# Performance work log

Measured on AMD Instinct MI355X. Metric: run time of the kernel, lower is better.

The kernel has to match this reference:

```python
import jax, jax.numpy as jnp
import numpy as np

B, N_LAT, N_CTX, DIM = 4, 512, 4096, 512
HEADS, DIM_HEAD = 8, 64
DIM_INNER = HEADS * DIM_HEAD  # 512


def setup_inputs() -> dict:
    key = jax.random.key(0)
    k1, k2, k3, k4, k5 = jax.random.split(key, 5)
    x = jax.random.normal(k1, (B, N_LAT, DIM), dtype=jnp.float32)
    context = jax.random.normal(k2, (B, N_CTX, DIM), dtype=jnp.float32)
    # eqx.nn.Linear weights have shape (out_features, in_features); scale ~ 1/sqrt(in)
    s = 1.0 / np.sqrt(DIM)
    Wq = jax.random.normal(k3, (DIM_INNER, DIM), dtype=jnp.float32) * s
    Wkv = jax.random.normal(k4, (2 * DIM_INNER, DIM), dtype=jnp.float32) * s
    Wout = jax.random.normal(k5, (DIM, DIM_INNER), dtype=jnp.float32) * (1.0 / np.sqrt(DIM_INNER))
    return {"x": x, "context": context, "Wq": Wq, "Wkv": Wkv, "Wout": Wout}


def reference(x, context, Wq, Wkv, Wout):
    h, d = HEADS, DIM_HEAD
    # queries are prepended to the context (unconditional in the source)
    ctx = jnp.concatenate([x, context], axis=1)              # [b, n+m, dim]
    q = jnp.einsum('bnd,ed->bne', x, Wq)                     # [b, n, h*d]
    kv = jnp.einsum('bmd,ed->bme', ctx, Wkv)                 # [b, n+m, 2*h*d]
    k, v = jnp.split(kv, 2, axis=-1)
    # b n (h d) -> b h n d
    def split_heads(t):
        b, n, _ = t.shape
        return t.reshape(b, n, h, d).transpose(0, 2, 1, 3)
    q, k, v = split_heads(q), split_heads(k), split_heads(v)
    scale = d ** (-0.5)
    scores = jnp.einsum('bhnd,bhmd->bhnm', q, k) * scale     # [b, h, n, n+m]
    attn = jax.nn.softmax(scores, axis=-1)
    out = jnp.einsum('bhnm,bhmd->bhnd', attn, v)             # [b, h, n, d]
    b, _, n, _ = out.shape
    out = out.transpose(0, 2, 1, 3).reshape(b, n, h * d)     # b h n d -> b n (h d)
    return jnp.einsum('bne,de->bnd', out, Wout)
```

## Files before the change

kernel.cpp:

```cpp
#include <hip/hip_runtime.h>
#include <hip/hip_bf16.h>
#include <cstdint>

#define DEVI __device__ __forceinline__

typedef unsigned short u16;
typedef unsigned int u32;
typedef __attribute__((ext_vector_type(8))) short bf16x8;
typedef __attribute__((ext_vector_type(4))) float f32x4;
typedef __attribute__((ext_vector_type(4))) int i32x4;

DEVI u16 f2bf(float f) {
    union { float f; u32 u; } v; v.f = f;
    u32 r = v.u + 0x7fffu + ((v.u >> 16) & 1u);
    return (u16)(r >> 16);
}
DEVI u32 pk2(float a, float b) { return (u32)f2bf(a) | ((u32)f2bf(b) << 16); }

DEVI u32 cvtpk_bf16(float lo, float hi) {
    u32 r;
    asm("v_cvt_pk_bf16_f32 %0, %1, %2" : "=v"(r) : "v"(lo), "v"(hi));
    return r;
}

DEVI void gload_lds16(const void* g, void* l) {
    __builtin_amdgcn_global_load_lds(
        (const __attribute__((address_space(1))) u32*)(uintptr_t)g,
        (__attribute__((address_space(3))) u32*)(u32)(uintptr_t)l,
        16, 0, 0);
}

__global__ __launch_bounds__(256) void prep_all(const float* __restrict__ x,
                                                const float* __restrict__ ctx,
                                                const float* __restrict__ Wq,
                                                const float* __restrict__ Wkv,
                                                const float* __restrict__ Wout,
                                                u16* __restrict__ ctxb,
                                                u16* __restrict__ wqb,
                                                u16* __restrict__ wkvb,
                                                u16* __restrict__ woutb) {
    int id = blockIdx.x;
    int tid = threadIdx.x;
    if (id < 4608) {
        int idx = id * 256 + tid;
        long e0 = (long)idx * 8;
        int b = (int)(e0 / (4608L * 512));
        long rem = e0 % (4608L * 512);
        int m = (int)(rem / 512);
        int d = (int)(rem % 512);
        const float* src = (m < 512) ? (x + ((long)b * 512 + m) * 512 + d)
                                     : (ctx + ((long)b * 4096 + (m - 512)) * 512 + d);
        float4 a = *(const float4*)src;
        float4 c = *(const float4*)(src + 4);
        uint4 u;
        u.x = pk2(a.x, a.y); u.y = pk2(a.z, a.w);
        u.z = pk2(c.x, c.y); u.w = pk2(c.z, c.w);
        *(uint4*)&ctxb[e0] = u;
        return;
    }
    const float* s;
    u16* d;
    int i;
    if (id < 4736)      { s = Wq;   d = wqb;   i = (id - 4608) * 256 + tid; }
    else if (id < 4992) { s = Wkv;  d = wkvb;  i = (id - 4736) * 256 + tid; }
    else                { s = Wout; d = woutb; i = (id - 4992) * 256 + tid; }
    const float4* s4 = (const float4*)s;
    float4 a = s4[i * 2], b = s4[i * 2 + 1];
    uint4 u;
    u.x = pk2(a.x, a.y); u.y = pk2(a.z, a.w);
    u.z = pk2(b.x, b.y); u.w = pk2(b.z, b.w);
    ((uint4*)d)[i] = u;
}

__global__ __launch_bounds__(512) void gemm_kvq(const u16* __restrict__ ctxb,
                                                const u16* __restrict__ wkvb,
                                                const u16* __restrict__ wqb,
                                                u16* __restrict__ kb,
                                                u16* __restrict__ vtb,
                                                u16* __restrict__ qb) {
    const int K = 512;
    __shared__ u16 Asm[2][128 * 64];
    __shared__ u16 Bsm[2][256 * 64];
    int tid = threadIdx.x;
    int w = tid >> 6, l = tid & 63;
    int g = l >> 4, c = l & 15;
    int wr = w >> 2, wc = w & 3;

    const u16* B;
    u16* C;
    long r0, arow0;
    int rpb;
    bool isq = (blockIdx.y >= 144);
    if (isq) {
        if (blockIdx.x >= 2) return;
        r0 = (long)(blockIdx.y - 144) * 128;
        rpb = 512;
        B = wqb;
        C = qb;
    } else {
        r0 = (long)blockIdx.y * 128;
        rpb = 4608;
        B = wkvb;
        C = kb;
    }
    arow0 = (r0 / rpb) * (4608L * 512) + (r0 % rpb) * K;
    int n0 = blockIdx.x * 256;

    f32x4 acc[4][4];
#pragma unroll
    for (int i = 0; i < 4; i++)
#pragma unroll
        for (int j = 0; j < 4; j++) acc[i][j] = (f32x4){0.f, 0.f, 0.f, 0.f};

    int srow = l >> 3;
    int sch = l & 7;

    auto stage = [&](int kt, int bb) {
#pragma unroll
        for (int i = 0; i < 2; i++) {
            int c2 = w * 2 + i;
            int row = c2 * 8 + srow;
            int sc = sch ^ (row & 7);
            gload_lds16(ctxb + arow0 + (long)row * K + kt * 64 + sc * 8,
                        &Asm[bb][c2 * 512 + (l << 3)]);
        }
#pragma unroll
        for (int i = 0; i < 4; i++) {
            int c2 = w * 4 + i;
            int row = c2 * 8 + srow;
            int sc = sch ^ (row & 7);
            gload_lds16(B + (long)(n0 + row) * K + kt * 64 + sc * 8,
                        &Bsm[bb][c2 * 512 + (l << 3)]);
        }
    };

    stage(0, 0);
#pragma unroll 2
    for (int kt = 0; kt < 8; ++kt) {
        int pb = kt & 1;
        if (kt < 7) {
            stage(kt + 1, pb ^ 1);
            asm volatile("s_waitcnt vmcnt(6)" ::: "memory");
        } else {
            asm volatile("s_waitcnt vmcnt(0)" ::: "memory");
        }
        __builtin_amdgcn_s_barrier();
        __builtin_amdgcn_sched_barrier(0);
#pragma unroll
        for (int ks = 0; ks < 2; ++ks) {
            bf16x8 af[4], bfr[4];
#pragma unroll
            for (int mt = 0; mt < 4; ++mt) {
                int row = wr * 64 + mt * 16 + c;
                int ch = (ks * 4 + g) ^ (row & 7);
                af[mt] = *(const bf16x8*)&Asm[pb][row * 64 + ch * 8];
            }
#pragma unroll
            for (int nt = 0; nt < 4; ++nt) {
                int row = wc * 64 + nt * 16 + c;
                int ch = (ks * 4 + g) ^ (row & 7);
                bfr[nt] = *(const bf16x8*)&Bsm[pb][row * 64 + ch * 8];
            }
            __builtin_amdgcn_s_setprio(1);
#pragma unroll
            for (int mt = 0; mt < 4; ++mt)
#pragma unroll
                for (int nt = 0; nt < 4; ++nt)
                    acc[mt][nt] = __builtin_amdgcn_mfma_f32_16x16x32_bf16(
                        af[mt], bfr[nt], acc[mt][nt], 0, 0, 0);
            __builtin_amdgcn_s_setprio(0);
        }
        __builtin_amdgcn_s_barrier();
    }

    if (!isq && n0 >= 512) {
        int b2 = (int)(r0 / 4608);
        int mb = (int)(r0 - (long)b2 * 4608) + wr * 64;
#pragma unroll
        for (int mt = 0; mt < 4; ++mt) {
#pragma unroll
            for (int nt = 0; nt < 4; ++nt) {
                int colv = (n0 - 512) + wc * 64 + nt * 16 + c;
                int hh = colv >> 6, dd = colv & 63;
                long ob = ((long)(b2 * 8 + hh) * 64 + dd) * 4608 + mb + mt * 16 + g * 4;
                ushort4 pk;
                pk.x = f2bf(acc[mt][nt][0]);
                pk.y = f2bf(acc[mt][nt][1]);
                pk.z = f2bf(acc[mt][nt][2]);
                pk.w = f2bf(acc[mt][nt][3]);
                *(ushort4*)&vtb[ob] = pk;
            }
        }
        return;
    }
#pragma unroll
    for (int mt = 0; mt < 4; ++mt) {
#pragma unroll
        for (int r = 0; r < 4; ++r) {
            long row = r0 + wr * 64 + mt * 16 + g * 4 + r;
#pragma unroll
            for (int nt = 0; nt < 4; ++nt) {
                int col = n0 + wc * 64 + nt * 16 + c;
                C[row * 512 + col] = f2bf(acc[mt][nt][r]);
            }
        }
    }
}

__global__ __launch_bounds__(256) void gemm_out(const u16* __restrict__ A,
                                                const u16* __restrict__ B,
                                                float* __restrict__ C) {
    const int K = 512;
    __shared__ u16 Asm[2][64 * 64];
    __shared__ u16 Bsm[2][128 * 64];
    int tid = threadIdx.x;
    int w = tid >> 6, l = tid & 63;
    int g = l >> 4, c = l & 15;
    int wr = w >> 1, wc = w & 1;
    long r0 = (long)blockIdx.y * 64;
    long arow0 = r0 * K;
    int n0 = blockIdx.x * 128;

    f32x4 acc[2][4];
#pragma unroll
    for (int i = 0; i < 2; i++)
#pragma unroll
        for (int j = 0; j < 4; j++) acc[i][j] = (f32x4){0.f, 0.f, 0.f, 0.f};

    int srow = l >> 3;
    int sch = l & 7;

    auto stage = [&](int kt, int bb) {
#pragma unroll
        for (int i = 0; i < 2; i++) {
            int c2 = w * 2 + i;
            int row = c2 * 8 + srow;
            int sc = sch ^ (row & 7);
            gload_lds16(A + arow0 + (long)row * K + kt * 64 + sc * 8,
                        &Asm[bb][c2 * 512 + (l << 3)]);
        }
#pragma unroll
        for (int i = 0; i < 4; i++) {
            int c2 = w * 4 + i;
            int row = c2 * 8 + srow;
            int sc = sch ^ (row & 7);
            gload_lds16(B + (long)(n0 + row) * K + kt * 64 + sc * 8,
                        &Bsm[bb][c2 * 512 + (l << 3)]);
        }
    };

    stage(0, 0);
#pragma unroll 2
    for (int kt = 0; kt < 8; ++kt) {
        int pb = kt & 1;
        if (kt < 7) {
            stage(kt + 1, pb ^ 1);
            asm volatile("s_waitcnt vmcnt(6)" ::: "memory");
        } else {
            asm volatile("s_waitcnt vmcnt(0)" ::: "memory");
        }
        __builtin_amdgcn_s_barrier();
        __builtin_amdgcn_sched_barrier(0);
#pragma unroll
        for (int ks = 0; ks < 2; ++ks) {
            bf16x8 af[2], bfr[4];
#pragma unroll
            for (int mt = 0; mt < 2; ++mt) {
                int row = wr * 32 + mt * 16 + c;
                int ch = (ks * 4 + g) ^ (row & 7);
                af[mt] = *(const bf16x8*)&Asm[pb][row * 64 + ch * 8];
            }
#pragma unroll
            for (int nt = 0; nt < 4; ++nt) {
                int row = wc * 64 + nt * 16 + c;
                int ch = (ks * 4 + g) ^ (row & 7);
                bfr[nt] = *(const bf16x8*)&Bsm[pb][row * 64 + ch * 8];
            }
#pragma unroll
            for (int mt = 0; mt < 2; ++mt)
#pragma unroll
                for (int nt = 0; nt < 4; ++nt)
                    acc[mt][nt] = __builtin_amdgcn_mfma_f32_16x16x32_bf16(
                        af[mt], bfr[nt], acc[mt][nt], 0, 0, 0);
        }
        __builtin_amdgcn_s_barrier();
    }
#pragma unroll
    for (int mt = 0; mt < 2; ++mt) {
#pragma unroll
        for (int r = 0; r < 4; ++r) {
            long row = r0 + wr * 32 + mt * 16 + g * 4 + r;
#pragma unroll
            for (int nt = 0; nt < 4; ++nt) {
                int col = n0 + wc * 64 + nt * 16 + c;
                C[row * 512 + col] = acc[mt][nt][r];
            }
        }
    }
}

__global__ __launch_bounds__(256) void attn_kern(const u16* __restrict__ Q,
                                                 const u16* __restrict__ KB,
                                                 const u16* __restrict__ VT,
                                                 float* __restrict__ Op,
                                                 float2* __restrict__ ML) {
    __shared__ u16 Ksm[2][64 * 64];
    __shared__ u16 Vsm[2][64 * 64];
    int tid = threadIdx.x;
    int w = tid >> 6, l = tid & 63;
    int g = l >> 4, c = l & 15;
    int id = blockIdx.x;
    int u = (id & 7) | ((id >> 6) << 3);
    int qi = (id >> 3) & 7;
    int p_ = u >> 3, chunk = u & 7;
    int b = p_ >> 3, h = p_ & 7;
    int qb0 = qi * 64;
    const int NT = 9;
    int it0 = chunk * NT;

    bf16x8 qf[2];
    {
        long qrow = (long)(b * 512 + qb0 + w * 16 + c);
#pragma unroll
        for (int ks = 0; ks < 2; ++ks)
            qf[ks] = *(const bf16x8*)&Q[qrow * 512 + h * 64 + ks * 32 + g * 8];
    }
    f32x4 o[4];
#pragma unroll
    for (int nt = 0; nt < 4; nt++) o[nt] = (f32x4){0.f, 0.f, 0.f, 0.f};
    float mrun = -1e30f, lrun = 0.f;

    const float SCL = 0.125f * 1.44269504f;
    int srow8 = l >> 3, sch = l & 7;
    const long kbase = (long)b * 4608 * 512 + h * 64;
    const long vtbase = (long)(b * 8 + h) * 64 * 4608;

    int g2 = g << 1;
    int srcA = ((g2 & 3) << 4) | c;
    int srcB = (((g2 | 1) & 3) << 4) | c;
    bool hiT2 = (g >> 1) != 0;

    auto stage = [&](int it, int bb) {
#pragma unroll
        for (int i = 0; i < 2; i++) {
            int c2 = w * 2 + i;
            int row = c2 * 8 + srow8;
            int sc = sch ^ (row & 7);
            gload_lds16(KB + kbase + (long)(it * 64 + row) * 512 + sc * 8,
                        &Ksm[bb][c2 * 512 + (l << 3)]);
            gload_lds16(VT + vtbase + (long)row * 4608 + it * 64 + sc * 8,
                        &Vsm[bb][c2 * 512 + (l << 3)]);
        }
    };

    stage(it0, 0);
    for (int t = 0; t < NT; ++t) {
        int pbuf = t & 1;
        if (t + 1 < NT) {
            stage(it0 + t + 1, pbuf ^ 1);
            asm volatile("s_waitcnt vmcnt(4)" ::: "memory");
        } else {
            asm volatile("s_waitcnt vmcnt(0)" ::: "memory");
        }
        __builtin_amdgcn_s_barrier();
        __builtin_amdgcn_sched_barrier(0);

        f32x4 st[4];
#pragma unroll
        for (int t2 = 0; t2 < 4; t2++) st[t2] = (f32x4){0.f, 0.f, 0.f, 0.f};
        __builtin_amdgcn_s_setprio(1);
#pragma unroll
        for (int ks = 0; ks < 2; ++ks) {
#pragma unroll
            for (int t2 = 0; t2 < 4; t2++) {
                int row = t2 * 16 + c;
                int ch = (ks * 4 + g) ^ (row & 7);
                bf16x8 kf = *(const bf16x8*)&Ksm[pbuf][row * 64 + ch * 8];
                st[t2] = __builtin_amdgcn_mfma_f32_16x16x32_bf16(kf, qf[ks], st[t2], 0, 0, 0);
            }
        }
        __builtin_amdgcn_s_setprio(0);

        float mx01 = fmaxf(fmaxf(st[0][0], st[0][1]), fmaxf(st[0][2], st[0][3]));
        float mx23 = fmaxf(fmaxf(st[1][0], st[1][1]), fmaxf(st[1][2], st[1][3]));
        float mx45 = fmaxf(fmaxf(st[2][0], st[2][1]), fmaxf(st[2][2], st[2][3]));
        float mx67 = fmaxf(fmaxf(st[3][0], st[3][1]), fmaxf(st[3][2], st[3][3]));
        float mx = fmaxf(fmaxf(mx01, mx23), fmaxf(mx45, mx67)) * SCL;
        mx = fmaxf(mx, __shfl_xor(mx, 16));
        mx = fmaxf(mx, __shfl_xor(mx, 32));

        bool need = mx > mrun + 8.f;
        if (__ballot(need)) {
            float mnew = fmaxf(mrun, mx);
            float rf = exp2f(mrun - mnew);
            mrun = mnew;
            lrun *= rf;
#pragma unroll
            for (int nt = 0; nt < 4; nt++)
#pragma unroll
                for (int r = 0; r < 4; r++) o[nt][r] *= rf;
        }
#pragma unroll
        for (int t2 = 0; t2 < 4; t2++)
#pragma unroll
            for (int r = 0; r < 4; r++) st[t2][r] = exp2f(st[t2][r] * SCL - mrun);

        lrun += ((st[0][0] + st[0][1]) + (st[0][2] + st[0][3]))
              + ((st[1][0] + st[1][1]) + (st[1][2] + st[1][3]))
              + ((st[2][0] + st[2][1]) + (st[2][2] + st[2][3]))
              + ((st[3][0] + st[3][1]) + (st[3][2] + st[3][3]));

        u32 u01[4], u23[4];
#pragma unroll
        for (int t2 = 0; t2 < 4; t2++) {
            u01[t2] = cvtpk_bf16(st[t2][0], st[t2][1]);
            u23[t2] = cvtpk_bf16(st[t2][2], st[t2][3]);
        }
        bf16x8 pbf[2];
#pragma unroll
        for (int ks = 0; ks < 2; ++ks) {
            u32 a0 = (u32)__shfl((int)u01[2 * ks], srcA);
            u32 a1 = (u32)__shfl((int)u01[2 * ks + 1], srcA);
            u32 b0 = (u32)__shfl((int)u23[2 * ks], srcA);
            u32 b1 = (u32)__shfl((int)u23[2 * ks + 1], srcA);
            u32 c0 = (u32)__shfl((int)u01[2 * ks], srcB);
            u32 c1 = (u32)__shfl((int)u01[2 * ks + 1], srcB);
            u32 d0 = (u32)__shfl((int)u23[2 * ks], srcB);
            u32 d1 = (u32)__shfl((int)u23[2 * ks + 1], srcB);
            i32x4 vv;
            vv[0] = (int)(hiT2 ? a1 : a0);
            vv[1] = (int)(hiT2 ? b1 : b0);
            vv[2] = (int)(hiT2 ? c1 : c0);
            vv[3] = (int)(hiT2 ? d1 : d0);
            pbf[ks] = __builtin_bit_cast(bf16x8, vv);
        }

        __builtin_amdgcn_s_setprio(1);
#pragma unroll
        for (int ks = 0; ks < 2; ++ks) {
#pragma unroll
            for (int nt = 0; nt < 4; nt++) {
                int vrow = nt * 16 + c;
                int vch = (ks * 4 + g) ^ (vrow & 7);
                bf16x8 vb = *(const bf16x8*)&Vsm[pbuf][vrow * 64 + vch * 8];
                o[nt] = __builtin_amdgcn_mfma_f32_16x16x32_bf16(vb, pbf[ks], o[nt], 0, 0, 0);
            }
        }
        __builtin_amdgcn_s_setprio(0);
        __builtin_amdgcn_s_barrier();
    }

    lrun += __shfl_xor(lrun, 16);
    lrun += __shfl_xor(lrun, 32);

    long prow = (long)(chunk * 32 + p_) * 512 + qb0 + w * 16;
#pragma unroll
    for (int nt = 0; nt < 4; nt++)
        *(f32x4*)&Op[(prow + c) * 64 + nt * 16 + g * 4] = o[nt];
    if (g == 0) ML[prow + c] = make_float2(mrun, lrun);
}

__global__ __launch_bounds__(256) void attn_combine(const float* __restrict__ Op,
                                                    const float2* __restrict__ ML,
                                                    u16* __restrict__ O) {
    int tid = threadIdx.x;
    int w = tid >> 6, l = tid & 63;
    long rid = (long)blockIdx.x * 4 + w;
    int p_ = (int)(rid >> 9);
    int row = (int)(rid & 511);
    int b = p_ >> 3, h = p_ & 7;
    float2 m[8];
#pragma unroll
    for (int cc = 0; cc < 8; cc++) m[cc] = ML[((long)(cc * 32 + p_) * 512 + row)];
    float mstar = fmaxf(fmaxf(fmaxf(m[0].x, m[1].x), fmaxf(m[2].x, m[3].x)),
                        fmaxf(fmaxf(m[4].x, m[5].x), fmaxf(m[6].x, m[7].x)));
    float wsum = 0.f, acc = 0.f;
#pragma unroll
    for (int cc = 0; cc < 8; cc++) {
        float wgt = exp2f(m[cc].x - mstar);
        wsum += wgt * m[cc].y;
        acc += wgt * Op[((long)(cc * 32 + p_) * 512 + row) * 64 + l];
    }
    O[((long)(b * 512 + row)) * 512 + h * 64 + l] = f2bf(acc / wsum);
}


extern "C" void kernel_launch(void* const* d_in, const int* in_sizes, int n_in,
                              void* d_out, int out_size, void* d_ws, size_t ws_size,
                              hipStream_t stream) {
    const float* x = (const float*)d_in[0];
    const float* ctx = (const float*)d_in[1];
    const float* Wq = (const float*)d_in[2];
    const float* Wkv = (const float*)d_in[3];
    const float* Wout = (const float*)d_in[4];
    float* out = (float*)d_out;

    char* ws = (char*)d_ws;
    size_t off = 0;
    auto alloc = [&](size_t bytes) {
        size_t r = off;
        off += (bytes + 255) & ~(size_t)255;
        return r;
    };
    u16* ctxb = (u16*)(ws + alloc(4L * 4608 * 512 * 2));
    u16* wqb = (u16*)(ws + alloc(512L * 512 * 2));
    u16* wkvb = (u16*)(ws + alloc(1024L * 512 * 2));
    u16* woutb = (u16*)(ws + alloc(512L * 512 * 2));
    u16* qb = (u16*)(ws + alloc(2048L * 512 * 2));
    u16* kb = (u16*)(ws + alloc(4L * 4608 * 512 * 2));
    u16* vtb = (u16*)(ws + alloc(4L * 8 * 64 * 4608 * 2));
    u16* aob = (u16*)(ws + alloc(2048L * 512 * 2));
    float* opb = (float*)(ws + alloc(8L * 32 * 512 * 64 * 4));
    float2* mlb = (float2*)(ws + alloc(8L * 32 * 512 * 8));

    prep_all<<<dim3(5120), dim3(256), 0, stream>>>(x, ctx, Wq, Wkv, Wout,
                                                   ctxb, wqb, wkvb, woutb);
    gemm_kvq<<<dim3(4, 160), dim3(512), 0, stream>>>(ctxb, wkvb, wqb, kb, vtb, qb);
    attn_kern<<<dim3(2048), dim3(256), 0, stream>>>(qb, kb, vtb, opb, mlb);
    attn_combine<<<dim3(4096), dim3(256), 0, stream>>>(opb, mlb, aob);
    gemm_out<<<dim3(4, 32), dim3(256), 0, stream>>>(aob, woutb, out);
}
```

Baseline: 192.3 us.

## Permute V-transpose layout to drop P shuffles and double attention block size

The KV GEMM epilogue now writes V^T with a permuted column order within each 64-wide group, so the softmax probabilities' MFMA output layout matches the B-operand layout directly. This removes eight cross-lane shuffles and selects per k-step in the attention inner loop. Attention blocks grow from 256 to 512 threads covering 128 queries, so each staged K/V tile is shared by twice as many query rows, and each thread issues one load per tile instead of two. Larger blocks may reduce occupancy, and the layout change couples the GEMM epilogue and the attention kernel tightly.

Measured after the change: 175.7 us. 8.6% less time.

```diff
diff --git a/kernel.cpp b/kernel.cpp
--- a/kernel.cpp
+++ b/kernel.cpp
@@ -182,7 +182,8 @@
             for (int nt = 0; nt < 4; ++nt) {
                 int colv = (n0 - 512) + wc * 64 + nt * 16 + c;
                 int hh = colv >> 6, dd = colv & 63;
-                long ob = ((long)(b2 * 8 + hh) * 64 + dd) * 4608 + mb + mt * 16 + g * 4;
+                long ob = ((long)(b2 * 8 + hh) * 64 + dd) * 4608 + mb
+                        + (mt >> 1) * 32 + g * 8 + (mt & 1) * 4;
                 ushort4 pk;
                 pk.x = f2bf(acc[mt][nt][0]);
                 pk.y = f2bf(acc[mt][nt][1]);
@@ -299,7 +300,7 @@
     }
 }
 
-__global__ __launch_bounds__(256) void attn_kern(const u16* __restrict__ Q,
+__global__ __launch_bounds__(512) void attn_kern(const u16* __restrict__ Q,
                                                  const u16* __restrict__ KB,
                                                  const u16* __restrict__ VT,
                                                  float* __restrict__ Op,
@@ -310,11 +311,11 @@
     int w = tid >> 6, l = tid & 63;
     int g = l >> 4, c = l & 15;
     int id = blockIdx.x;
-    int u = (id & 7) | ((id >> 6) << 3);
-    int qi = (id >> 3) & 7;
+    int u = (id & 7) | ((id >> 5) << 3);
+    int qi = (id >> 3) & 3;
     int p_ = u >> 3, chunk = u & 7;
     int b = p_ >> 3, h = p_ & 7;
-    int qb0 = qi * 64;
+    int qb0 = qi * 128;
     const int NT = 9;
     int it0 = chunk * NT;
 
@@ -331,26 +332,17 @@
     float mrun = -1e30f, lrun = 0.f;
 
     const float SCL = 0.125f * 1.44269504f;
-    int srow8 = l >> 3, sch = l & 7;
     const long kbase = (long)b * 4608 * 512 + h * 64;
     const long vtbase = (long)(b * 8 + h) * 64 * 4608;
 
-    int g2 = g << 1;
-    int srcA = ((g2 & 3) << 4) | c;
-    int srcB = (((g2 | 1) & 3) << 4) | c;
-    bool hiT2 = (g >> 1) != 0;
+    int srow = tid >> 3;
+    int ssc = (tid & 7) ^ (srow & 7);
 
     auto stage = [&](int it, int bb) {
-#pragma unroll
-        for (int i = 0; i < 2; i++) {
-            int c2 = w * 2 + i;
-            int row = c2 * 8 + srow8;
-            int sc = sch ^ (row & 7);
-            gload_lds16(KB + kbase + (long)(it * 64 + row) * 512 + sc * 8,
-                        &Ksm[bb][c2 * 512 + (l << 3)]);
-            gload_lds16(VT + vtbase + (long)row * 4608 + it * 64 + sc * 8,
-                        &Vsm[bb][c2 * 512 + (l << 3)]);
-        }
+        gload_lds16(KB + kbase + (long)(it * 64 + srow) * 512 + ssc * 8,
+                    &Ksm[bb][tid * 8]);
+        gload_lds16(VT + vtbase + (long)srow * 4608 + it * 64 + ssc * 8,
+                    &Vsm[bb][tid * 8]);
     };
 
     stage(it0, 0);
@@ -358,7 +350,7 @@
         int pbuf = t & 1;
         if (t + 1 < NT) {
             stage(it0 + t + 1, pbuf ^ 1);
-            asm volatile("s_waitcnt vmcnt(4)" ::: "memory");
+            asm volatile("s_waitcnt vmcnt(2)" ::: "memory");
         } else {
             asm volatile("s_waitcnt vmcnt(0)" ::: "memory");
         }
@@ -410,28 +402,14 @@
               + ((st[2][0] + st[2][1]) + (st[2][2] + st[2][3]))
               + ((st[3][0] + st[3][1]) + (st[3][2] + st[3][3]));
 
-        u32 u01[4], u23[4];
-#pragma unroll
-        for (int t2 = 0; t2 < 4; t2++) {
-            u01[t2] = cvtpk_bf16(st[t2][0], st[t2][1]);
-            u23[t2] = cvtpk_bf16(st[t2][2], st[t2][3]);
-        }
         bf16x8 pbf[2];
 #pragma unroll
         for (int ks = 0; ks < 2; ++ks) {
-            u32 a0 = (u32)__shfl((int)u01[2 * ks], srcA);
-            u32 a1 = (u32)__shfl((int)u01[2 * ks + 1], srcA);
-            u32 b0 = (u32)__shfl((int)u23[2 * ks], srcA);
-            u32 b1 = (u32)__shfl((int)u23[2 * ks + 1], srcA);
-            u32 c0 = (u32)__shfl((int)u01[2 * ks], srcB);
-            u32 c1 = (u32)__shfl((int)u01[2 * ks + 1], srcB);
-            u32 d0 = (u32)__shfl((int)u23[2 * ks], srcB);
-            u32 d1 = (u32)__shfl((int)u23[2 * ks + 1], srcB);
             i32x4 vv;
-            vv[0] = (int)(hiT2 ? a1 : a0);
-            vv[1] = (int)(hiT2 ? b1 : b0);
-            vv[2] = (int)(hiT2 ? c1 : c0);
-            vv[3] = (int)(hiT2 ? d1 : d0);
+            vv[0] = (int)cvtpk_bf16(st[2 * ks][0], st[2 * ks][1]);
+            vv[1] = (int)cvtpk_bf16(st[2 * ks][2], st[2 * ks][3]);
+            vv[2] = (int)cvtpk_bf16(st[2 * ks + 1][0], st[2 * ks + 1][1]);
+            vv[3] = (int)cvtpk_bf16(st[2 * ks + 1][2], st[2 * ks + 1][3]);
             pbf[ks] = __builtin_bit_cast(bf16x8, vv);
         }
 
@@ -516,7 +494,7 @@
     prep_all<<<dim3(5120), dim3(256), 0, stream>>>(x, ctx, Wq, Wkv, Wout,
                                                    ctxb, wqb, wkvb, woutb);
     gemm_kvq<<<dim3(4, 160), dim3(512), 0, stream>>>(ctxb, wkvb, wqb, kb, vtb, qb);
-    attn_kern<<<dim3(2048), dim3(256), 0, stream>>>(qb, kb, vtb, opb, mlb);
+    attn_kern<<<dim3(1024), dim3(512), 0, stream>>>(qb, kb, vtb, opb, mlb);
     attn_combine<<<dim3(4096), dim3(256), 0, stream>>>(opb, mlb, aob);
     gemm_out<<<dim3(4, 32), dim3(256), 0, stream>>>(aob, woutb, out);
 }
```
